# Kernel tuning notes

Measured on AMD Instinct MI355X. Metric: run time of the kernel, lower is better.

The kernel has to match this reference:

```python
import jax, jax.numpy as jnp
import numpy as np
from jax import lax
import math

D_MODEL = 768
D_SSM = 1536      # expand * d_model
D_STATE = 128
D_CONV = 4
HEADDIM = 64
NHEADS = D_SSM // HEADDIM          # 24
CONV_DIM = D_SSM + 2 * D_STATE     # 1792 (ngroups=1)
D_IN_PROJ = 2 * D_SSM + 2 * D_STATE + NHEADS  # 3352
BATCH, SEQLEN = 4, 2048
EPS = 1e-5


def setup_inputs() -> dict:
    key = jax.random.key(0)
    ks = jax.random.split(key, 10)
    u = jax.random.normal(ks[0], (BATCH, SEQLEN, D_MODEL), dtype=jnp.float32)
    W_in = jax.random.normal(ks[1], (D_IN_PROJ, D_MODEL), dtype=jnp.float32) * (1.0 / math.sqrt(D_MODEL))
    conv_w = jax.random.normal(ks[2], (CONV_DIM, D_CONV), dtype=jnp.float32) * (1.0 / math.sqrt(D_CONV))
    conv_b = jax.random.normal(ks[3], (CONV_DIM,), dtype=jnp.float32) * 0.02
    # dt_bias init as in torch code
    dt = jnp.exp(jax.random.uniform(ks[4], (NHEADS,)) * (math.log(0.1) - math.log(0.001)) + math.log(0.001))
    dt = jnp.clip(dt, 1e-4, None)
    dt_bias = dt + jnp.log(-jnp.expm1(-dt))
    A_log = jnp.log(jax.random.uniform(ks[5], (NHEADS,), minval=1.0, maxval=16.0))
    D = jnp.ones((NHEADS,), dtype=jnp.float32)
    norm_w = jnp.ones((D_SSM,), dtype=jnp.float32)
    W_out = jax.random.normal(ks[6], (D_MODEL, D_SSM), dtype=jnp.float32) * (1.0 / math.sqrt(D_SSM))
    return {"u": u, "W_in": W_in, "conv_w": conv_w, "conv_b": conv_b,
            "dt_bias": dt_bias, "A_log": A_log, "D": D, "norm_w": norm_w, "W_out": W_out}


def _mamba2(u, W_in, conv_w, conv_b, dt_bias, A_log, D, norm_w, W_out):
    B_, L, _ = u.shape
    zxbcdt = jnp.einsum('bld,ed->ble', u, W_in)  # [B, L, 3352]
    z = zxbcdt[..., :D_SSM]
    xBC = zxbcdt[..., D_SSM:D_SSM + CONV_DIM]
    dt_raw = zxbcdt[..., D_SSM + CONV_DIM:]      # [B, L, H]

    # causal depthwise conv1d + silu
    xBC_t = jnp.transpose(xBC, (0, 2, 1))        # [B, C, L]
    conv = lax.conv_general_dilated(
        xBC_t, conv_w[:, None, :], window_strides=(1,),
        padding=[(D_CONV - 1, 0)], feature_group_count=CONV_DIM,
        dimension_numbers=('NCH', 'OIH', 'NCH'))
    conv = conv + conv_b[None, :, None]
    xBC = jnp.transpose(jax.nn.silu(conv), (0, 2, 1))  # [B, L, C]

    x = xBC[..., :D_SSM].reshape(B_, L, NHEADS, HEADDIM)
    Bm = xBC[..., D_SSM:D_SSM + D_STATE]         # [B, L, N] (ngroups=1)
    Cm = xBC[..., D_SSM + D_STATE:]              # [B, L, N]

    dt = jax.nn.softplus(dt_raw + dt_bias)       # [B, L, H]
    A = -jnp.exp(A_log)                          # [H]

    def step(h, inp):
        dt_t, x_t, B_t, C_t = inp                # [B,H], [B,H,P], [B,N], [B,N]
        dA = jnp.exp(dt_t * A)                   # [B,H]
        h = h * dA[..., None, None] + jnp.einsum('bh,bhp,bn->bhpn', dt_t, x_t, B_t)
        y_t = jnp.einsum('bhpn,bn->bhp', h, C_t)
        return h, y_t

    h0 = jnp.zeros((B_, NHEADS, HEADDIM, D_STATE), dtype=u.dtype)
    xs = (jnp.transpose(dt, (1, 0, 2)), jnp.transpose(x, (1, 0, 2, 3)),
          jnp.transpose(Bm, (1, 0, 2)), jnp.transpose(Cm, (1, 0, 2)))
    _, ys = lax.scan(step, h0, xs)               # ys: [L, B, H, P]
    y = jnp.transpose(ys, (1, 0, 2, 3)) + D[None, None, :, None] * x
    y = y.reshape(B_, L, D_SSM)

    # RMSNormGated with norm_before_gate=False: normalize after gating
    yz = y * jax.nn.silu(z)
    yn = yz * lax.rsqrt(jnp.mean(yz * yz, axis=-1, keepdims=True) + EPS) * norm_w
    return jnp.einsum('ble,de->bld', yn, W_out)  # [B, L, d_model]


def reference(u, W_in, conv_w, conv_b, dt_bias, A_log, D, norm_w, W_out):
    return _mamba2(u, W_in, conv_w, conv_b, dt_bias, A_log, D, norm_w, W_out)
```

## Files before the change

kernel.cpp:

```cpp
#include <hip/hip_runtime.h>
#include <hip/hip_bf16.h>
#include <math.h>

#define D_MODEL   768
#define D_SSM     1536
#define D_STATE   128
#define D_CONV    4
#define HEADDIM   64
#define NHEADS    24
#define CONV_DIM  1792
#define D_IN_PROJ 3352
#define BATCH     4
#define SEQLEN    2048
#define NROWS     (BATCH * SEQLEN)
#define EPS       1e-5f

#define CHUNK     64
#define NC        (SEQLEN / CHUNK)
#define NBH       (BATCH * NHEADS)
#define HSTATE    (HEADDIM * D_STATE)

#define K3_IN     (3 * D_MODEL)
#define K3_OUT    (3 * D_SSM)
#define NPAD_IN   3456

typedef __attribute__((ext_vector_type(8))) short bf16x8;
typedef __attribute__((ext_vector_type(4))) float f32x4;

__device__ __forceinline__ float sigmoidf_(float x) {
    return 1.0f / (1.0f + __expf(-x));
}

__device__ __forceinline__ void gload16(void* lds, const void* g) {
    __builtin_amdgcn_global_load_lds(
        (const __attribute__((address_space(1))) unsigned int*)g,
        (__attribute__((address_space(3))) unsigned int*)lds, 16, 0, 0);
}

__device__ __forceinline__ void cvt_wr8(__hip_bfloat16* hb, __hip_bfloat16* lb,
                                        int off, float4 a, float4 b)
{
    union { __hip_bfloat16 h[8]; uint4 u; } hi, lo;
    const float f[8] = {a.x, a.y, a.z, a.w, b.x, b.y, b.z, b.w};
#pragma unroll
    for (int j = 0; j < 8; ++j) {
        const __hip_bfloat16 h = __float2bfloat16(f[j]);
        hi.h[j] = h;
        lo.h[j] = __float2bfloat16(f[j] - __bfloat162float(h));
    }
    *(uint4*)((char*)hb + off) = hi.u;
    *(uint4*)((char*)lb + off) = lo.u;
}

template<int APAT>
__global__ __launch_bounds__(256) void decompose3(
    const float* __restrict__ X, __hip_bfloat16* __restrict__ X3,
    int R, int Rpad, int K)
{
    const int idx = blockIdx.x * 256 + threadIdx.x;
    if (idx >= Rpad * (K / 4)) return;
    const int r = idx / (K / 4);
    const int k = (idx % (K / 4)) * 4;

    union { __hip_bfloat16 h[4]; uint2 u; } phi, plo;
    if (r < R) {
        const float4 x = *(const float4*)(X + (size_t)r * K + k);
        const float xs[4] = {x.x, x.y, x.z, x.w};
#pragma unroll
        for (int j = 0; j < 4; ++j) {
            phi.h[j] = __float2bfloat16(xs[j]);
            plo.h[j] = __float2bfloat16(xs[j] - __bfloat162float(phi.h[j]));
        }
    } else {
#pragma unroll
        for (int j = 0; j < 4; ++j) { phi.h[j] = __float2bfloat16(0.f); plo.h[j] = phi.h[j]; }
    }
    __hip_bfloat16* row = X3 + (size_t)r * (3 * K);
    *(uint2*)(row + k)         = phi.u;
    *(uint2*)(row + K + k)     = APAT ? phi.u : plo.u;
    *(uint2*)(row + 2 * K + k) = APAT ? plo.u : phi.u;
}

template<int MODE>
__global__ __launch_bounds__(256) void gemm_bf16x3(
    const __hip_bfloat16* __restrict__ Ab, const __hip_bfloat16* __restrict__ Bb,
    float* __restrict__ C0, float* __restrict__ C1, float* __restrict__ C2,
    int Nreal, int K3)
{
    __shared__ __hip_bfloat16 Asm[2][128][32];
    __shared__ __hip_bfloat16 Bsm[2][128][32];
    const int tid  = threadIdx.x;
    const int lane = tid & 63;
    const int w    = tid >> 6;
    const int wr   = w >> 1, wc = w & 1;
    const int bm   = blockIdx.y * 128;
    const int bn   = blockIdx.x * 128;

    const __hip_bfloat16* gA[2];
    const __hip_bfloat16* gB[2];
    int ldsrow[2];
#pragma unroll
    for (int i = 0; i < 2; ++i) {
        const int r  = w * 32 + i * 16 + (lane >> 2);
        const int sl = (lane & 3) ^ ((r ^ (r >> 2)) & 3);
        ldsrow[i] = w * 32 + i * 16;
        gA[i] = Ab + (size_t)(bm + r) * K3 + sl * 8;
        gB[i] = Bb + (size_t)(bn + r) * K3 + sl * 8;
    }

    int aoff[4], boff[4];
#pragma unroll
    for (int mi = 0; mi < 4; ++mi) {
        const int ra = wr * 64 + mi * 16 + (lane & 15);
        aoff[mi] = ra * 64 + (((lane >> 4) ^ ((ra ^ (ra >> 2)) & 3)) << 4);
        const int rb = wc * 64 + mi * 16 + (lane & 15);
        boff[mi] = rb * 64 + (((lane >> 4) ^ ((rb ^ (rb >> 2)) & 3)) << 4);
    }

    f32x4 acc[4][4] = {};

    const int nk = K3 / 32;
#pragma unroll
    for (int i = 0; i < 2; ++i) {
        gload16(&Asm[0][ldsrow[i]][0], gA[i]);
        gload16(&Bsm[0][ldsrow[i]][0], gB[i]);
    }
    __syncthreads();

    int buf = 0;
    for (int kt = 0; kt < nk; ++kt) {
        if (kt + 1 < nk) {
            const int ko = (kt + 1) * 32;
#pragma unroll
            for (int i = 0; i < 2; ++i) {
                gload16(&Asm[buf ^ 1][ldsrow[i]][0], gA[i] + ko);
                gload16(&Bsm[buf ^ 1][ldsrow[i]][0], gB[i] + ko);
            }
        }
        const char* ab = (const char*)&Asm[buf][0][0];
        const char* bb = (const char*)&Bsm[buf][0][0];
        bf16x8 afr[4], bfr[4];
#pragma unroll
        for (int i = 0; i < 4; ++i) {
            afr[i] = *(const bf16x8*)(ab + aoff[i]);
            bfr[i] = *(const bf16x8*)(bb + boff[i]);
        }
#pragma unroll
        for (int mi = 0; mi < 4; ++mi)
#pragma unroll
            for (int ni = 0; ni < 4; ++ni)
                acc[mi][ni] = __builtin_amdgcn_mfma_f32_16x16x32_bf16(
                    afr[mi], bfr[ni], acc[mi][ni], 0, 0, 0);
        __syncthreads();
        buf ^= 1;
    }

#pragma unroll
    for (int mi = 0; mi < 4; ++mi) {
        const int rn = bm + wr * 64 + mi * 16 + ((lane >> 4) << 2);
#pragma unroll
        for (int ni = 0; ni < 4; ++ni) {
            const int cn = bn + wc * 64 + ni * 16 + (lane & 15);
#pragma unroll
            for (int j = 0; j < 4; ++j) {
                const float v = acc[mi][ni][j];
                const int r = rn + j;
                if (MODE == 0) {
                    C0[(size_t)r * Nreal + cn] = v;
                } else {
                    if (cn < D_SSM)                 C0[(size_t)r * D_SSM + cn] = v;
                    else if (cn < D_SSM + CONV_DIM) C1[(size_t)r * CONV_DIM + (cn - D_SSM)] = v;
                    else if (cn < D_IN_PROJ)        C2[(size_t)r * NHEADS + (cn - D_SSM - CONV_DIM)] = v;
                }
            }
        }
    }
}

template<int BM, int BN, int BK>
__global__ __launch_bounds__(256) void gemm_nt(
    const float* __restrict__ A, const float* __restrict__ B,
    float* __restrict__ C, int M, int N, int K)
{
    __shared__ float As[BK][BM];
    __shared__ float Bs[BK][BN];
    const int tid = threadIdx.x;
    const int bm  = blockIdx.y * BM;
    const int bn  = blockIdx.x * BN;
    const int tm  = (tid & 15) << 2;
    const int tn  = (tid >> 4) << 2;
    const int am  = tid & 63;
    const int ak  = (tid >> 6) << 2;
    float acc[4][4] = {};
    for (int k0 = 0; k0 < K; k0 += BK) {
        const float4 av = *(const float4*)(A + (size_t)(bm + am) * K + (k0 + ak));
        float4 bv = make_float4(0.f, 0.f, 0.f, 0.f);
        if (bn + am < N)
            bv = *(const float4*)(B + (size_t)(bn + am) * K + (k0 + ak));
        __syncthreads();
        As[ak + 0][am] = av.x; As[ak + 1][am] = av.y;
        As[ak + 2][am] = av.z; As[ak + 3][am] = av.w;
        Bs[ak + 0][am] = bv.x; Bs[ak + 1][am] = bv.y;
        Bs[ak + 2][am] = bv.z; Bs[ak + 3][am] = bv.w;
        __syncthreads();
#pragma unroll
        for (int kk = 0; kk < BK; ++kk) {
            const float4 a4 = *(const float4*)&As[kk][tm];
            const float4 b4 = *(const float4*)&Bs[kk][tn];
            const float a[4]  = {a4.x, a4.y, a4.z, a4.w};
            const float bb[4] = {b4.x, b4.y, b4.z, b4.w};
#pragma unroll
            for (int i = 0; i < 4; ++i)
#pragma unroll
                for (int j = 0; j < 4; ++j)
                    acc[i][j] = fmaf(a[i], bb[j], acc[i][j]);
        }
    }
#pragma unroll
    for (int i = 0; i < 4; ++i)
#pragma unroll
        for (int j = 0; j < 4; ++j) {
            const int cn = bn + tn + j;
            if (cn < N)
                C[(size_t)(bm + tm + i) * N + cn] = acc[i][j];
        }
}

__global__ __launch_bounds__(256) void gemm_inproj(
    const float* __restrict__ A, const float* __restrict__ B,
    float* __restrict__ zbuf, float* __restrict__ xbc, float* __restrict__ dtraw)
{
    constexpr int BM = 64, BN = 64, BK = 16;
    __shared__ float As[BK][BM];
    __shared__ float Bs[BK][BN];
    const int tid = threadIdx.x;
    const int bm  = blockIdx.y * BM;
    const int bn  = blockIdx.x * BN;
    const int tm  = (tid & 15) << 2;
    const int tn  = (tid >> 4) << 2;
    const int am  = tid & 63;
    const int ak  = (tid >> 6) << 2;
    float acc[4][4] = {};
    for (int k0 = 0; k0 < D_MODEL; k0 += BK) {
        const float4 av = *(const float4*)(A + (size_t)(bm + am) * D_MODEL + (k0 + ak));
        float4 bv = make_float4(0.f, 0.f, 0.f, 0.f);
        if (bn + am < D_IN_PROJ)
            bv = *(const float4*)(B + (size_t)(bn + am) * D_MODEL + (k0 + ak));
        __syncthreads();
        As[ak + 0][am] = av.x; As[ak + 1][am] = av.y;
        As[ak + 2][am] = av.z; As[ak + 3][am] = av.w;
        Bs[ak + 0][am] = bv.x; Bs[ak + 1][am] = bv.y;
        Bs[ak + 2][am] = bv.z; Bs[ak + 3][am] = bv.w;
        __syncthreads();
#pragma unroll
        for (int kk = 0; kk < BK; ++kk) {
            const float4 a4 = *(const float4*)&As[kk][tm];
            const float4 b4 = *(const float4*)&Bs[kk][tn];
            const float a[4]  = {a4.x, a4.y, a4.z, a4.w};
            const float bb[4] = {b4.x, b4.y, b4.z, b4.w};
#pragma unroll
            for (int i = 0; i < 4; ++i)
#pragma unroll
                for (int j = 0; j < 4; ++j)
                    acc[i][j] = fmaf(a[i], bb[j], acc[i][j]);
        }
    }
    float* Cp; int ldc, cb, nlim = BN;
    if (bn < D_SSM)                  { Cp = zbuf;  ldc = D_SSM;    cb = bn; }
    else if (bn < D_SSM + CONV_DIM)  { Cp = xbc;   ldc = CONV_DIM; cb = bn - D_SSM; }
    else { Cp = dtraw; ldc = NHEADS; cb = bn - (D_SSM + CONV_DIM); nlim = NHEADS; }
#pragma unroll
    for (int i = 0; i < 4; ++i)
#pragma unroll
        for (int j = 0; j < 4; ++j)
            if (tn + j < nlim)
                Cp[(size_t)(bm + tm + i) * ldc + cb + tn + j] = acc[i][j];
}

__global__ __launch_bounds__(256) void conv_silu_kernel(
    const float* __restrict__ xbc, const float* __restrict__ cw,
    const float* __restrict__ cb, float* __restrict__ xc)
{
    const int idx = blockIdx.x * 256 + threadIdx.x;
    if (idx >= NROWS * (CONV_DIM / 4)) return;
    const int row = idx / (CONV_DIM / 4);
    const int c   = (idx % (CONV_DIM / 4)) * 4;
    const int l   = row & (SEQLEN - 1);

    const float* base = xbc + (size_t)row * CONV_DIM + c;
    const float4 cbv = *(const float4*)(cb + c);
    float acc[4] = {cbv.x, cbv.y, cbv.z, cbv.w};
    const float* w = cw + (size_t)c * D_CONV;
#pragma unroll
    for (int k = 0; k < D_CONV; ++k) {
        const int ls = l + k - 3;
        if (ls >= 0) {
            const float4 xv = *(const float4*)(base + (ptrdiff_t)(k - 3) * CONV_DIM);
            acc[0] = fmaf(w[0 * D_CONV + k], xv.x, acc[0]);
            acc[1] = fmaf(w[1 * D_CONV + k], xv.y, acc[1]);
            acc[2] = fmaf(w[2 * D_CONV + k], xv.z, acc[2]);
            acc[3] = fmaf(w[3 * D_CONV + k], xv.w, acc[3]);
        }
    }
    float4 o;
    o.x = acc[0] * sigmoidf_(acc[0]);
    o.y = acc[1] * sigmoidf_(acc[1]);
    o.z = acc[2] * sigmoidf_(acc[2]);
    o.w = acc[3] * sigmoidf_(acc[3]);
    *(float4*)(xc + (size_t)row * CONV_DIM + c) = o;
}

__global__ __launch_bounds__(64) void dt_kernel(
    const float* __restrict__ dtraw, const float* __restrict__ dt_bias,
    float* __restrict__ dtw)
{
    const int row = blockIdx.x;
    const int tid = threadIdx.x;
    if (tid < NHEADS) {
        const float x = dtraw[(size_t)row * NHEADS + tid] + dt_bias[tid];
        const float sp = fmaxf(x, 0.f) + log1pf(__expf(-fabsf(x)));
        dtw[(size_t)row * NHEADS + tid] = sp;
    }
}

__global__ __launch_bounds__(256) void chunk_state_kernel(
    const float* __restrict__ xc, const float* __restrict__ dtw,
    const float* __restrict__ A_log,
    float* __restrict__ Sbuf, float* __restrict__ cumws)
{
    const int c  = blockIdx.x / NBH;
    const int bh = blockIdx.x % NBH;
    const int b  = bh / NHEADS, h = bh % NHEADS;
    const int tid = threadIdx.x;
    const int rowbase = b * SEQLEN + c * CHUNK;

    __shared__ float cums[CHUNK];
    __shared__ float wls[CHUNK];
    __shared__ float Xw[CHUNK][HEADDIM];
    __shared__ float Bsh[CHUNK][D_STATE];

    const float Aneg = -__expf(A_log[h]);

    float dtv = 0.f;
    if (tid < CHUNK) dtv = dtw[(size_t)(rowbase + tid) * NHEADS + h];
    float v = Aneg * dtv;
#pragma unroll
    for (int d = 1; d < 64; d <<= 1) {
        const float o = __shfl_up(v, d);
        if ((tid & 63) >= d) v += o;
    }
    if (tid < CHUNK) {
        cums[tid] = v;
        cumws[(size_t)bh * SEQLEN + c * CHUNK + tid] = v;
    }
    __syncthreads();
    const float clast = cums[CHUNK - 1];
    if (tid < CHUNK) wls[tid] = __expf(clast - v) * dtv;
    __syncthreads();

    {
        const int p0 = (tid & 15) * 4, s0 = tid >> 4;
        for (int s = s0; s < CHUNK; s += 16) {
            const float4 xv = *(const float4*)(xc + (size_t)(rowbase + s) * CONV_DIM + h * HEADDIM + p0);
            const float w = wls[s];
            *(float4*)&Xw[s][p0] = make_float4(xv.x * w, xv.y * w, xv.z * w, xv.w * w);
        }
        const int n0 = (tid & 31) * 4, s1 = tid >> 5;
        for (int s = s1; s < CHUNK; s += 8)
            *(float4*)&Bsh[s][n0] = *(const float4*)(xc + (size_t)(rowbase + s) * CONV_DIM + D_SSM + n0);
    }
    __syncthreads();

    const int tp = (tid & 15) * 4;
    const int tn = (tid >> 4) * 8;
    float acc[4][8] = {};
    for (int s = 0; s < CHUNK; ++s) {
        const float4 xa = *(const float4*)&Xw[s][tp];
        const float4 b0 = *(const float4*)&Bsh[s][tn];
        const float4 b1 = *(const float4*)&Bsh[s][tn + 4];
        const float xr[4] = {xa.x, xa.y, xa.z, xa.w};
        const float br[8] = {b0.x, b0.y, b0.z, b0.w, b1.x, b1.y, b1.z, b1.w};
#pragma unroll
        for (int i = 0; i < 4; ++i)
#pragma unroll
            for (int j = 0; j < 8; ++j)
                acc[i][j] = fmaf(xr[i], br[j], acc[i][j]);
    }
    float* Sp = Sbuf + (size_t)(bh * NC + c) * HSTATE;
#pragma unroll
    for (int i = 0; i < 4; ++i) {
        *(float4*)(Sp + (size_t)(tp + i) * D_STATE + tn)     = make_float4(acc[i][0], acc[i][1], acc[i][2], acc[i][3]);
        *(float4*)(Sp + (size_t)(tp + i) * D_STATE + tn + 4) = make_float4(acc[i][4], acc[i][5], acc[i][6], acc[i][7]);
    }
}

__global__ __launch_bounds__(256) void state_scan_kernel(
    const float* __restrict__ cumws, float* __restrict__ Sbuf)
{
    const int bh = blockIdx.x;
    const int e  = blockIdx.y * 256 + threadIdx.x;
    float* base = Sbuf + (size_t)bh * NC * HSTATE + e;
    const float* cw = cumws + (size_t)bh * SEQLEN;
    float H = 0.f;
    for (int c = 0; c < NC; ++c) {
        const float P = __expf(cw[c * CHUNK + CHUNK - 1]);
        const float s = base[(size_t)c * HSTATE];
        base[(size_t)c * HSTATE] = H;
        H = fmaf(P, H, s);
    }
}

__global__ __launch_bounds__(256) void chunk_output_mfma(
    const float* __restrict__ xc, const float* __restrict__ dtw,
    const float* __restrict__ Dp,
    const float* __restrict__ Hbuf, const float* __restrict__ cumws,
    float* __restrict__ y)
{
    const int c  = blockIdx.x / NBH;
    const int bh = blockIdx.x % NBH;
    const int b  = bh / NHEADS, h = bh % NHEADS;
    const int tid  = threadIdx.x;
    const int lane = tid & 63;
    const int w    = tid >> 6;
    const int rowbase = b * SEQLEN + c * CHUNK;

    __shared__ float s_cums[CHUNK], s_dts[CHUNK], s_Es[CHUNK];
    __shared__ __align__(16) __hip_bfloat16 Chi[CHUNK][D_STATE];
    __shared__ __align__(16) __hip_bfloat16 Clo[CHUNK][D_STATE];
    __shared__ __align__(16) __hip_bfloat16 BHhi[CHUNK][D_STATE];
    __shared__ __align__(16) __hip_bfloat16 BHlo[CHUNK][D_STATE];
    __shared__ __align__(16) __hip_bfloat16 Mhi[CHUNK][CHUNK];
    __shared__ __align__(16) __hip_bfloat16 Mlo[CHUNK][CHUNK];
    __shared__ __align__(16) __hip_bfloat16 XThi[CHUNK][CHUNK];
    __shared__ __align__(16) __hip_bfloat16 XTlo[CHUNK][CHUNK];

    float4 cv[4][2], bvv[4][2];
#pragma unroll
    for (int k = 0; k < 4; ++k) {
        const int q = tid + k * 256;
        const int row = q >> 4, slot = q & 15;
        const float* rp = xc + (size_t)(rowbase + row) * CONV_DIM + D_SSM;
        bvv[k][0] = *(const float4*)(rp + slot * 8);
        bvv[k][1] = *(const float4*)(rp + slot * 8 + 4);
        cv[k][0]  = *(const float4*)(rp + D_STATE + slot * 8);
        cv[k][1]  = *(const float4*)(rp + D_STATE + slot * 8 + 4);
    }
    if (tid < CHUNK) {
        const float cu = cumws[(size_t)bh * SEQLEN + c * CHUNK + tid];
        s_cums[tid] = cu;
        s_Es[tid]   = __expf(cu);
        s_dts[tid]  = dtw[(size_t)(rowbase + tid) * NHEADS + h];
    }
#pragma unroll
    for (int k = 0; k < 4; ++k) {
        const int q = tid + k * 256;
        const int row = q >> 4, slot = q & 15;
        const int off = row * 256 + ((slot ^ (row & 7)) << 4);
        cvt_wr8(&Chi[0][0],  &Clo[0][0],  off, cv[k][0],  cv[k][1]);
        cvt_wr8(&BHhi[0][0], &BHlo[0][0], off, bvv[k][0], bvv[k][1]);
    }
    float4 hv[4][2];
#pragma unroll
    for (int k = 0; k < 4; ++k) {
        const int q = tid + k * 256;
        const int p = q >> 4, slot = q & 15;
        const float* hp = Hbuf + (size_t)(bh * NC + c) * HSTATE + (size_t)p * D_STATE + slot * 8;
        hv[k][0] = *(const float4*)hp;
        hv[k][1] = *(const float4*)(hp + 4);
    }
    float4 xv[4];
#pragma unroll
    for (int k = 0; k < 4; ++k) {
        const int q = tid + k * 256;
        const int s = q >> 4, p4 = (q & 15) * 4;
        xv[k] = *(const float4*)(xc + (size_t)(rowbase + s) * CONV_DIM + h * HEADDIM + p4);
    }
    __syncthreads();

    const int fr = lane & 15;
    const int fs = lane >> 4;
    const int rA = w * 16 + fr;

    f32x4 g[4] = {};
#pragma unroll
    for (int pass = 0; pass < 3; ++pass) {
        const char* Ab = (const char*)(pass == 2 ? &Clo[0][0]  : &Chi[0][0]);
        const char* Bb = (const char*)(pass == 1 ? &BHlo[0][0] : &BHhi[0][0]);
#pragma unroll
        for (int kt = 0; kt < 4; ++kt) {
            const bf16x8 af = *(const bf16x8*)(Ab + rA * 256 + (((kt * 4 + fs) ^ (rA & 7)) << 4));
#pragma unroll
            for (int nt = 0; nt < 4; ++nt) {
                const int rb = nt * 16 + fr;
                const bf16x8 bf = *(const bf16x8*)(Bb + rb * 256 + (((kt * 4 + fs) ^ (rb & 7)) << 4));
                g[nt] = __builtin_amdgcn_mfma_f32_16x16x32_bf16(af, bf, g[nt], 0, 0, 0);
            }
        }
    }

    const float Dh = Dp[h];
#pragma unroll
    for (int nt = 0; nt < 4; ++nt) {
        const int s = nt * 16 + fr;
#pragma unroll
        for (int j = 0; j < 4; ++j) {
            const int t = w * 16 + fs * 4 + j;
            float m = 0.f;
            if (s <= t) {
                m = g[nt][j] * __expf(s_cums[t] - s_cums[s]) * s_dts[s];
                if (s == t) m += Dh;
            }
            const __hip_bfloat16 mh = __float2bfloat16(m);
            const __hip_bfloat16 ml = __float2bfloat16(m - __bfloat162float(mh));
            const int moff = t * 128 + ((((s >> 3) ^ (t & 7))) << 4) + ((s & 7) << 1);
            *(__hip_bfloat16*)((char*)&Mhi[0][0] + moff) = mh;
            *(__hip_bfloat16*)((char*)&Mlo[0][0] + moff) = ml;
        }
    }
    __syncthreads();

#pragma unroll
    for (int k = 0; k < 4; ++k) {
        const int q = tid + k * 256;
        const int p = q >> 4, slot = q & 15;
        const int off = p * 256 + ((slot ^ (p & 7)) << 4);
        cvt_wr8(&BHhi[0][0], &BHlo[0][0], off, hv[k][0], hv[k][1]);
    }
#pragma unroll
    for (int k = 0; k < 4; ++k) {
        const int q = tid + k * 256;
        const int s = q >> 4, p4 = (q & 15) * 4;
        const float f[4] = {xv[k].x, xv[k].y, xv[k].z, xv[k].w};
#pragma unroll
        for (int j = 0; j < 4; ++j) {
            const int p = p4 + j;
            const __hip_bfloat16 xh = __float2bfloat16(f[j]);
            const __hip_bfloat16 xl = __float2bfloat16(f[j] - __bfloat162float(xh));
            const int off = p * 128 + ((((s >> 3) ^ (p & 7))) << 4) + ((s & 7) << 1);
            *(__hip_bfloat16*)((char*)&XThi[0][0] + off) = xh;
            *(__hip_bfloat16*)((char*)&XTlo[0][0] + off) = xl;
        }
    }
    __syncthreads();

    f32x4 acc[4] = {};
#pragma unroll
    for (int pass = 0; pass < 3; ++pass) {
        const char* Ab = (const char*)(pass == 2 ? &Clo[0][0]  : &Chi[0][0]);
        const char* Bb = (const char*)(pass == 1 ? &BHlo[0][0] : &BHhi[0][0]);
#pragma unroll
        for (int kt = 0; kt < 4; ++kt) {
            const bf16x8 af = *(const bf16x8*)(Ab + rA * 256 + (((kt * 4 + fs) ^ (rA & 7)) << 4));
#pragma unroll
            for (int nt = 0; nt < 4; ++nt) {
                const int rp = nt * 16 + fr;
                const bf16x8 bf = *(const bf16x8*)(Bb + rp * 256 + (((kt * 4 + fs) ^ (rp & 7)) << 4));
                acc[nt] = __builtin_amdgcn_mfma_f32_16x16x32_bf16(af, bf, acc[nt], 0, 0, 0);
            }
        }
    }
#pragma unroll
    for (int nt = 0; nt < 4; ++nt)
#pragma unroll
        for (int j = 0; j < 4; ++j)
            acc[nt][j] *= s_Es[w * 16 + fs * 4 + j];

    const int rM = w * 16 + fr;
#pragma unroll
    for (int pass = 0; pass < 3; ++pass) {
        const char* Ab = (const char*)(pass == 2 ? &Mlo[0][0]  : &Mhi[0][0]);
        const char* Bb = (const char*)(pass == 1 ? &XTlo[0][0] : &XThi[0][0]);
#pragma unroll
        for (int kt = 0; kt < 2; ++kt) {
            const bf16x8 af = *(const bf16x8*)(Ab + rM * 128 + (((kt * 4 + fs) ^ (rM & 7)) << 4));
#pragma unroll
            for (int nt = 0; nt < 4; ++nt) {
                const int rp = nt * 16 + fr;
                const bf16x8 bf = *(const bf16x8*)(Bb + rp * 128 + (((kt * 4 + fs) ^ (rp & 7)) << 4));
                acc[nt] = __builtin_amdgcn_mfma_f32_16x16x32_bf16(af, bf, acc[nt], 0, 0, 0);
            }
        }
    }

#pragma unroll
    for (int nt = 0; nt < 4; ++nt) {
        const int p = nt * 16 + fr;
#pragma unroll
        for (int j = 0; j < 4; ++j) {
            const int t = w * 16 + fs * 4 + j;
            y[(size_t)(rowbase + t) * D_SSM + h * HEADDIM + p] = acc[nt][j];
        }
    }
}

__global__ __launch_bounds__(256) void scan_kernel(
    const float* __restrict__ xc, const float* __restrict__ dtw,
    const float* __restrict__ A_log, const float* __restrict__ Dp,
    float* __restrict__ y)
{
    const int b   = blockIdx.x / NHEADS;
    const int h   = blockIdx.x % NHEADS;
    const int tid = threadIdx.x;
    const int p   = tid >> 2;
    const int q   = tid & 3;

    __shared__ float dt_s[SEQLEN];
    __shared__ float Bs[4][36];
    __shared__ float Cs[4][36];
    __shared__ float xs[64];

    for (int i = tid; i < SEQLEN; i += 256)
        dt_s[i] = dtw[((size_t)b * SEQLEN + i) * NHEADS + h];

    const float Aneg = -__expf(A_log[h]);
    const float Dh   = Dp[h];

    float hst[32];
#pragma unroll
    for (int i = 0; i < 32; ++i) hst[i] = 0.f;

    const float* row0 = xc + (size_t)b * SEQLEN * CONV_DIM;
    float rBC = row0[D_SSM + tid];
    float rx  = (tid < 64) ? row0[h * HEADDIM + tid] : 0.f;

    for (int t = 0; t < SEQLEN; ++t) {
        __syncthreads();
        if (tid < 128) Bs[tid >> 5][tid & 31] = rBC;
        else           Cs[(tid >> 5) & 3][tid & 31] = rBC;
        if (tid < 64)  xs[tid] = rx;
        if (t + 1 < SEQLEN) {
            const float* rp = row0 + (size_t)(t + 1) * CONV_DIM;
            rBC = rp[D_SSM + tid];
            if (tid < 64) rx = rp[h * HEADDIM + tid];
        }
        __syncthreads();

        const float dtv = dt_s[t];
        const float dA  = __expf(dtv * Aneg);
        const float dtx = dtv * xs[p];
        float ysum = 0.f;
#pragma unroll
        for (int j4 = 0; j4 < 8; ++j4) {
            const float4 Bv = *(const float4*)&Bs[q][j4 * 4];
            const float4 Cv = *(const float4*)&Cs[q][j4 * 4];
            float* hp = &hst[j4 * 4];
            hp[0] = fmaf(hp[0], dA, dtx * Bv.x); ysum = fmaf(hp[0], Cv.x, ysum);
            hp[1] = fmaf(hp[1], dA, dtx * Bv.y); ysum = fmaf(hp[1], Cv.y, ysum);
            hp[2] = fmaf(hp[2], dA, dtx * Bv.z); ysum = fmaf(hp[2], Cv.z, ysum);
            hp[3] = fmaf(hp[3], dA, dtx * Bv.w); ysum = fmaf(hp[3], Cv.w, ysum);
        }
        ysum += __shfl_xor(ysum, 1);
        ysum += __shfl_xor(ysum, 2);
        if (q == 0)
            y[((size_t)b * SEQLEN + t) * D_SSM + h * HEADDIM + p] = ysum + Dh * xs[p];
    }
}

__global__ __launch_bounds__(256) void gatenorm_x3_kernel(
    const float* __restrict__ y, const float* __restrict__ zbuf,
    const float* __restrict__ norm_w, __hip_bfloat16* __restrict__ ybx3)
{
    const int row = blockIdx.x;
    const int tid = threadIdx.x;
    const float* yr = y + (size_t)row * D_SSM;
    const float* zr = zbuf + (size_t)row * D_SSM;

    float v[6];
    float ss = 0.f;
#pragma unroll
    for (int i = 0; i < 6; ++i) {
        const int e = tid + i * 256;
        const float yv = yr[e];
        const float zv = zr[e];
        const float g  = yv * (zv * sigmoidf_(zv));
        v[i] = g;
        ss = fmaf(g, g, ss);
    }
#pragma unroll
    for (int m = 1; m < 64; m <<= 1) ss += __shfl_xor(ss, m);
    __shared__ float ws[4];
    if ((tid & 63) == 0) ws[tid >> 6] = ss;
    __syncthreads();
    const float tot = ws[0] + ws[1] + ws[2] + ws[3];
    const float r = rsqrtf(tot * (1.0f / D_SSM) + EPS);
    __hip_bfloat16* orow = ybx3 + (size_t)row * K3_OUT;
#pragma unroll
    for (int i = 0; i < 6; ++i) {
        const int e = tid + i * 256;
        const float g = v[i] * r * norm_w[e];
        const __hip_bfloat16 hi = __float2bfloat16(g);
        const __hip_bfloat16 lo = __float2bfloat16(g - __bfloat162float(hi));
        orow[e] = hi;
        orow[D_SSM + e] = hi;
        orow[2 * D_SSM + e] = lo;
    }
}

__global__ __launch_bounds__(256) void gatenorm_kernel(
    float* y, const float* __restrict__ zbuf, const float* __restrict__ norm_w)
{
    const int row = blockIdx.x;
    const int tid = threadIdx.x;
    float* yr = y + (size_t)row * D_SSM;
    const float* zr = zbuf + (size_t)row * D_SSM;

    float v[6];
    float ss = 0.f;
#pragma unroll
    for (int i = 0; i < 6; ++i) {
        const int e = tid + i * 256;
        const float yv = yr[e];
        const float zv = zr[e];
        const float g  = yv * (zv * sigmoidf_(zv));
        v[i] = g;
        ss = fmaf(g, g, ss);
    }
#pragma unroll
    for (int m = 1; m < 64; m <<= 1) ss += __shfl_xor(ss, m);
    __shared__ float ws[4];
    if ((tid & 63) == 0) ws[tid >> 6] = ss;
    __syncthreads();
    const float tot = ws[0] + ws[1] + ws[2] + ws[3];
    const float r = rsqrtf(tot * (1.0f / D_SSM) + EPS);
#pragma unroll
    for (int i = 0; i < 6; ++i) {
        const int e = tid + i * 256;
        yr[e] = v[i] * r * norm_w[e];
    }
}

extern "C" void kernel_launch(void* const* d_in, const int* in_sizes, int n_in,
                              void* d_out, int out_size, void* d_ws, size_t ws_size,
                              hipStream_t stream)
{
    const float* u       = (const float*)d_in[0];
    const float* W_in    = (const float*)d_in[1];
    const float* conv_w  = (const float*)d_in[2];
    const float* conv_b  = (const float*)d_in[3];
    const float* dt_bias = (const float*)d_in[4];
    const float* A_log   = (const float*)d_in[5];
    const float* Dp      = (const float*)d_in[6];
    const float* norm_w  = (const float*)d_in[7];
    const float* W_out   = (const float*)d_in[8];
    float* out = (float*)d_out;

    const size_t SZ_Z   = (size_t)NROWS * D_SSM;
    const size_t SZ_XBC = (size_t)NROWS * CONV_DIM;
    const size_t SZ_DT  = (size_t)NROWS * NHEADS;
    const size_t SZ_S   = (size_t)NBH * NC * HSTATE;
    const size_t SZ_CUM = (size_t)NBH * SEQLEN;

    const size_t need_new = (SZ_Z + SZ_S + SZ_Z + SZ_XBC + SZ_DT + SZ_CUM) * sizeof(float);
    const bool use_new = ws_size >= need_new;

    if (use_new) {
        float* zbuf = (float*)d_ws;
        float* Breg = zbuf + SZ_Z;
        float* Creg = Breg + SZ_S;
        float* Xreg = Creg + SZ_Z;
        float* dtw   = Xreg + SZ_XBC;
        float* cumws = dtw + SZ_DT;

        float* xbc   = Breg;
        float* dtraw = Breg + SZ_XBC;
        float* Sbuf  = Breg;
        __hip_bfloat16* ybx3 = (__hip_bfloat16*)Breg;
        __hip_bfloat16* u3   = (__hip_bfloat16*)Creg;
        float* yb    = Creg;
        __hip_bfloat16* W_in3  = (__hip_bfloat16*)Xreg;
        float* xc    = Xreg;
        __hip_bfloat16* W_out3 = (__hip_bfloat16*)Xreg;

        decompose3<1><<<(NROWS * (D_MODEL / 4) + 255) / 256, 256, 0, stream>>>(
            u, u3, NROWS, NROWS, D_MODEL);
        decompose3<0><<<(NPAD_IN * (D_MODEL / 4) + 255) / 256, 256, 0, stream>>>(
            W_in, W_in3, D_IN_PROJ, NPAD_IN, D_MODEL);

        gemm_bf16x3<1><<<dim3(NPAD_IN / 128, NROWS / 128), 256, 0, stream>>>(
            u3, W_in3, zbuf, xbc, dtraw, 0, K3_IN);

        conv_silu_kernel<<<(NROWS * (CONV_DIM / 4) + 255) / 256, 256, 0, stream>>>(
            xbc, conv_w, conv_b, xc);

        dt_kernel<<<NROWS, 64, 0, stream>>>(dtraw, dt_bias, dtw);

        chunk_state_kernel<<<NBH * NC, 256, 0, stream>>>(xc, dtw, A_log, Sbuf, cumws);
        state_scan_kernel<<<dim3(NBH, HSTATE / 256), 256, 0, stream>>>(cumws, Sbuf);
        chunk_output_mfma<<<NBH * NC, 256, 0, stream>>>(xc, dtw, Dp, Sbuf, cumws, yb);

        decompose3<0><<<(D_MODEL * (D_SSM / 4) + 255) / 256, 256, 0, stream>>>(
            W_out, W_out3, D_MODEL, D_MODEL, D_SSM);

        gatenorm_x3_kernel<<<NROWS, 256, 0, stream>>>(yb, zbuf, norm_w, ybx3);

        gemm_bf16x3<0><<<dim3(D_MODEL / 128, NROWS / 128), 256, 0, stream>>>(
            ybx3, W_out3, out, nullptr, nullptr, D_MODEL, K3_OUT);
    } else {
        float* zbuf  = (float*)d_ws;
        float* Rp    = zbuf + SZ_Z;
        float* xbc   = Rp;
        float* yb    = Rp;
        float* dtraw = Rp + SZ_XBC;
        float* xc    = dtraw + SZ_DT;
        float* dtw   = xc + SZ_XBC;

        gemm_inproj<<<dim3((D_IN_PROJ + 63) / 64, NROWS / 64), 256, 0, stream>>>(
            u, W_in, zbuf, xbc, dtraw);
        conv_silu_kernel<<<(NROWS * (CONV_DIM / 4) + 255) / 256, 256, 0, stream>>>(
            xbc, conv_w, conv_b, xc);
        dt_kernel<<<NROWS, 64, 0, stream>>>(dtraw, dt_bias, dtw);
        scan_kernel<<<NBH, 256, 0, stream>>>(xc, dtw, A_log, Dp, yb);
        gatenorm_kernel<<<NROWS, 256, 0, stream>>>(yb, zbuf, norm_w);
        gemm_nt<64, 64, 16><<<dim3(D_MODEL / 64, NROWS / 64), 256, 0, stream>>>(
            yb, W_out, out, NROWS, D_MODEL, D_SSM);
    }
}
```

Baseline: 727.3 us.

## Use bf16x3 MFMA for chunk state, fuse softplus, swizzle GEMM block order

Replaces the scalar FP32 chunk-state outer-product kernel with a bf16 hi/lo three-pass MFMA version that keeps near-FP32 accuracy. The separate dt softplus kernel is removed; softplus is now recomputed inside the chunk-state and chunk-output kernels, which saves a launch and a buffer round trip. The GEMM grid becomes 1D with a block-index swizzle that spreads consecutive blocks across XCDs, aimed at better L2 locality. Side effects are extra bf16 conversion work and some redundant softplus evaluation.

```diff
diff --git a/kernel.cpp b/kernel.cpp
--- a/kernel.cpp
+++ b/kernel.cpp
@@ -31,6 +31,10 @@
     return 1.0f / (1.0f + __expf(-x));
 }
 
+__device__ __forceinline__ float softplusf_(float x) {
+    return fmaxf(x, 0.f) + log1pf(__expf(-fabsf(x)));
+}
+
 __device__ __forceinline__ void gload16(void* lds, const void* g) {
     __builtin_amdgcn_global_load_lds(
         (const __attribute__((address_space(1))) unsigned int*)g,
@@ -85,7 +89,7 @@
 __global__ __launch_bounds__(256) void gemm_bf16x3(
     const __hip_bfloat16* __restrict__ Ab, const __hip_bfloat16* __restrict__ Bb,
     float* __restrict__ C0, float* __restrict__ C1, float* __restrict__ C2,
-    int Nreal, int K3)
+    int Nreal, int K3, int nx)
 {
     __shared__ __hip_bfloat16 Asm[2][128][32];
     __shared__ __hip_bfloat16 Bsm[2][128][32];
@@ -93,8 +97,11 @@
     const int lane = tid & 63;
     const int w    = tid >> 6;
     const int wr   = w >> 1, wc = w & 1;
-    const int bm   = blockIdx.y * 128;
-    const int bn   = blockIdx.x * 128;
+
+    const int cpx = gridDim.x >> 3;
+    const int swz = (blockIdx.x & 7) * cpx + (blockIdx.x >> 3);
+    const int bm  = (swz / nx) * 128;
+    const int bn  = (swz % nx) * 128;
 
     const __hip_bfloat16* gA[2];
     const __hip_bfloat16* gB[2];
@@ -316,81 +323,123 @@
 {
     const int row = blockIdx.x;
     const int tid = threadIdx.x;
-    if (tid < NHEADS) {
-        const float x = dtraw[(size_t)row * NHEADS + tid] + dt_bias[tid];
-        const float sp = fmaxf(x, 0.f) + log1pf(__expf(-fabsf(x)));
-        dtw[(size_t)row * NHEADS + tid] = sp;
-    }
-}
-
-__global__ __launch_bounds__(256) void chunk_state_kernel(
-    const float* __restrict__ xc, const float* __restrict__ dtw,
-    const float* __restrict__ A_log,
+    if (tid < NHEADS)
+        dtw[(size_t)row * NHEADS + tid] = softplusf_(dtraw[(size_t)row * NHEADS + tid] + dt_bias[tid]);
+}
+
+__global__ __launch_bounds__(256) void chunk_state_mfma(
+    const float* __restrict__ xc, const float* __restrict__ dtraw,
+    const float* __restrict__ dt_bias, const float* __restrict__ A_log,
     float* __restrict__ Sbuf, float* __restrict__ cumws)
 {
     const int c  = blockIdx.x / NBH;
     const int bh = blockIdx.x % NBH;
     const int b  = bh / NHEADS, h = bh % NHEADS;
-    const int tid = threadIdx.x;
+    const int tid  = threadIdx.x;
+    const int lane = tid & 63;
+    const int w    = tid >> 6;
     const int rowbase = b * SEQLEN + c * CHUNK;
 
-    __shared__ float cums[CHUNK];
-    __shared__ float wls[CHUNK];
-    __shared__ float Xw[CHUNK][HEADDIM];
-    __shared__ float Bsh[CHUNK][D_STATE];
-
-    const float Aneg = -__expf(A_log[h]);
-
-    float dtv = 0.f;
-    if (tid < CHUNK) dtv = dtw[(size_t)(rowbase + tid) * NHEADS + h];
-    float v = Aneg * dtv;
-#pragma unroll
-    for (int d = 1; d < 64; d <<= 1) {
-        const float o = __shfl_up(v, d);
-        if ((tid & 63) >= d) v += o;
-    }
+    __shared__ float s_wls[CHUNK];
+    __shared__ __align__(16) __hip_bfloat16 Ahi[CHUNK][CHUNK];
+    __shared__ __align__(16) __hip_bfloat16 Alo[CHUNK][CHUNK];
+    __shared__ __align__(16) __hip_bfloat16 Bhi[D_STATE][CHUNK];
+    __shared__ __align__(16) __hip_bfloat16 Blo[D_STATE][CHUNK];
+
+    float4 bv[8];
+#pragma unroll
+    for (int k = 0; k < 8; ++k) {
+        const int q = tid + k * 256;
+        const int s = q >> 5, n4 = (q & 31) * 4;
+        bv[k] = *(const float4*)(xc + (size_t)(rowbase + s) * CONV_DIM + D_SSM + n4);
+    }
+    float4 xv[4];
+#pragma unroll
+    for (int k = 0; k < 4; ++k) {
+        const int q = tid + k * 256;
+        const int s = q >> 4, p4 = (q & 15) * 4;
+        xv[k] = *(const float4*)(xc + (size_t)(rowbase + s) * CONV_DIM + h * HEADDIM + p4);
+    }
+
     if (tid < CHUNK) {
-        cums[tid] = v;
+        const float Aneg = -__expf(A_log[h]);
+        const float dtv = softplusf_(dtraw[(size_t)(rowbase + tid) * NHEADS + h] + dt_bias[h]);
+        float v = Aneg * dtv;
+#pragma unroll
+        for (int d = 1; d < 64; d <<= 1) {
+            const float o = __shfl_up(v, d);
+            if (lane >= d) v += o;
+        }
         cumws[(size_t)bh * SEQLEN + c * CHUNK + tid] = v;
+        const float clast = __shfl(v, 63);
+        s_wls[tid] = __expf(clast - v) * dtv;
+    }
+
+#pragma unroll
+    for (int k = 0; k < 8; ++k) {
+        const int q = tid + k * 256;
+        const int s = q >> 5, n4 = (q & 31) * 4;
+        const float f[4] = {bv[k].x, bv[k].y, bv[k].z, bv[k].w};
+#pragma unroll
+        for (int j = 0; j < 4; ++j) {
+            const int n = n4 + j;
+            const __hip_bfloat16 hh = __float2bfloat16(f[j]);
+            const __hip_bfloat16 ll = __float2bfloat16(f[j] - __bfloat162float(hh));
+            const int off = n * 128 + ((((s >> 3) ^ (n & 7))) << 4) + ((s & 7) << 1);
+            *(__hip_bfloat16*)((char*)&Bhi[0][0] + off) = hh;
+            *(__hip_bfloat16*)((char*)&Blo[0][0] + off) = ll;
+        }
     }
     __syncthreads();
-    const float clast = cums[CHUNK - 1];
-    if (tid < CHUNK) wls[tid] = __expf(clast - v) * dtv;
+
+#pragma unroll
+    for (int k = 0; k < 4; ++k) {
+        const int q = tid + k * 256;
+        const int s = q >> 4, p4 = (q & 15) * 4;
+        const float wl = s_wls[s];
+        const float f[4] = {xv[k].x * wl, xv[k].y * wl, xv[k].z * wl, xv[k].w * wl};
+#pragma unroll
+        for (int j = 0; j < 4; ++j) {
+            const int p = p4 + j;
+            const __hip_bfloat16 hh = __float2bfloat16(f[j]);
+            const __hip_bfloat16 ll = __float2bfloat16(f[j] - __bfloat162float(hh));
+            const int off = p * 128 + ((((s >> 3) ^ (p & 7))) << 4) + ((s & 7) << 1);
+            *(__hip_bfloat16*)((char*)&Ahi[0][0] + off) = hh;
+            *(__hip_bfloat16*)((char*)&Alo[0][0] + off) = ll;
+        }
+    }
     __syncthreads();
 
-    {
-        const int p0 = (tid & 15) * 4, s0 = tid >> 4;
-        for (int s = s0; s < CHUNK; s += 16) {
-            const float4 xv = *(const float4*)(xc + (size_t)(rowbase + s) * CONV_DIM + h * HEADDIM + p0);
-            const float w = wls[s];
-            *(float4*)&Xw[s][p0] = make_float4(xv.x * w, xv.y * w, xv.z * w, xv.w * w);
-        }
-        const int n0 = (tid & 31) * 4, s1 = tid >> 5;
-        for (int s = s1; s < CHUNK; s += 8)
-            *(float4*)&Bsh[s][n0] = *(const float4*)(xc + (size_t)(rowbase + s) * CONV_DIM + D_SSM + n0);
-    }
-    __syncthreads();
-
-    const int tp = (tid & 15) * 4;
-    const int tn = (tid >> 4) * 8;
-    float acc[4][8] = {};
-    for (int s = 0; s < CHUNK; ++s) {
-        const float4 xa = *(const float4*)&Xw[s][tp];
-        const float4 b0 = *(const float4*)&Bsh[s][tn];
-        const float4 b1 = *(const float4*)&Bsh[s][tn + 4];
-        const float xr[4] = {xa.x, xa.y, xa.z, xa.w};
-        const float br[8] = {b0.x, b0.y, b0.z, b0.w, b1.x, b1.y, b1.z, b1.w};
-#pragma unroll
-        for (int i = 0; i < 4; ++i)
-#pragma unroll
-            for (int j = 0; j < 8; ++j)
-                acc[i][j] = fmaf(xr[i], br[j], acc[i][j]);
-    }
+    const int fr = lane & 15;
+    const int fs = lane >> 4;
+    const int rA = w * 16 + fr;
+    f32x4 acc[8] = {};
+#pragma unroll
+    for (int pass = 0; pass < 3; ++pass) {
+        const char* Ab = (const char*)(pass == 2 ? &Alo[0][0] : &Ahi[0][0]);
+        const char* Bb = (const char*)(pass == 1 ? &Blo[0][0] : &Bhi[0][0]);
+#pragma unroll
+        for (int kh = 0; kh < 2; ++kh) {
+            const int sl = kh * 4 + fs;
+            const bf16x8 af = *(const bf16x8*)(Ab + rA * 128 + ((sl ^ (rA & 7)) << 4));
+#pragma unroll
+            for (int nt = 0; nt < 8; ++nt) {
+                const int rB = nt * 16 + fr;
+                const bf16x8 bf = *(const bf16x8*)(Bb + rB * 128 + ((sl ^ (rB & 7)) << 4));
+                acc[nt] = __builtin_amdgcn_mfma_f32_16x16x32_bf16(af, bf, acc[nt], 0, 0, 0);
+            }
+        }
+    }
+
     float* Sp = Sbuf + (size_t)(bh * NC + c) * HSTATE;
 #pragma unroll
-    for (int i = 0; i < 4; ++i) {
-        *(float4*)(Sp + (size_t)(tp + i) * D_STATE + tn)     = make_float4(acc[i][0], acc[i][1], acc[i][2], acc[i][3]);
-        *(float4*)(Sp + (size_t)(tp + i) * D_STATE + tn + 4) = make_float4(acc[i][4], acc[i][5], acc[i][6], acc[i][7]);
+    for (int nt = 0; nt < 8; ++nt) {
+        const int n = nt * 16 + fr;
+#pragma unroll
+        for (int j = 0; j < 4; ++j) {
+            const int p = w * 16 + fs * 4 + j;
+            Sp[(size_t)p * D_STATE + n] = acc[nt][j];
+        }
     }
 }
 
@@ -411,8 +460,8 @@
 }
 
 __global__ __launch_bounds__(256) void chunk_output_mfma(
-    const float* __restrict__ xc, const float* __restrict__ dtw,
-    const float* __restrict__ Dp,
+    const float* __restrict__ xc, const float* __restrict__ dtraw,
+    const float* __restrict__ dt_bias, const float* __restrict__ Dp,
     const float* __restrict__ Hbuf, const float* __restrict__ cumws,
     float* __restrict__ y)
 {
@@ -449,7 +498,7 @@
         const float cu = cumws[(size_t)bh * SEQLEN + c * CHUNK + tid];
         s_cums[tid] = cu;
         s_Es[tid]   = __expf(cu);
-        s_dts[tid]  = dtw[(size_t)(rowbase + tid) * NHEADS + h];
+        s_dts[tid]  = softplusf_(dtraw[(size_t)(rowbase + tid) * NHEADS + h] + dt_bias[h]);
     }
 #pragma unroll
     for (int k = 0; k < 4; ++k) {
@@ -758,11 +807,10 @@
         float* Breg = zbuf + SZ_Z;
         float* Creg = Breg + SZ_S;
         float* Xreg = Creg + SZ_Z;
-        float* dtw   = Xreg + SZ_XBC;
-        float* cumws = dtw + SZ_DT;
+        float* dtraw = Xreg + SZ_XBC;
+        float* cumws = dtraw + SZ_DT;
 
         float* xbc   = Breg;
-        float* dtraw = Breg + SZ_XBC;
         float* Sbuf  = Breg;
         __hip_bfloat16* ybx3 = (__hip_bfloat16*)Breg;
         __hip_bfloat16* u3   = (__hip_bfloat16*)Creg;
@@ -776,25 +824,25 @@
         decompose3<0><<<(NPAD_IN * (D_MODEL / 4) + 255) / 256, 256, 0, stream>>>(
             W_in, W_in3, D_IN_PROJ, NPAD_IN, D_MODEL);
 
-        gemm_bf16x3<1><<<dim3(NPAD_IN / 128, NROWS / 128), 256, 0, stream>>>(
-            u3, W_in3, zbuf, xbc, dtraw, 0, K3_IN);
+        gemm_bf16x3<1><<<(NPAD_IN / 128) * (NROWS / 128), 256, 0, stream>>>(
+            u3, W_in3, zbuf, xbc, dtraw, 0, K3_IN, NPAD_IN / 128);
 
         conv_silu_kernel<<<(NROWS * (CONV_DIM / 4) + 255) / 256, 256, 0, stream>>>(
             xbc, conv_w, conv_b, xc);
 
-        dt_kernel<<<NROWS, 64, 0, stream>>>(dtraw, dt_bias, dtw);
-
-        chunk_state_kernel<<<NBH * NC, 256, 0, stream>>>(xc, dtw, A_log, Sbuf, cumws);
+        chunk_state_mfma<<<NBH * NC, 256, 0, stream>>>(
+            xc, dtraw, dt_bias, A_log, Sbuf, cumws);
         state_scan_kernel<<<dim3(NBH, HSTATE / 256), 256, 0, stream>>>(cumws, Sbuf);
-        chunk_output_mfma<<<NBH * NC, 256, 0, stream>>>(xc, dtw, Dp, Sbuf, cumws, yb);
+        chunk_output_mfma<<<NBH * NC, 256, 0, stream>>>(
+            xc, dtraw, dt_bias, Dp, Sbuf, cumws, yb);
 
         decompose3<0><<<(D_MODEL * (D_SSM / 4) + 255) / 256, 256, 0, stream>>>(
             W_out, W_out3, D_MODEL, D_MODEL, D_SSM);
 
         gatenorm_x3_kernel<<<NROWS, 256, 0, stream>>>(yb, zbuf, norm_w, ybx3);
 
-        gemm_bf16x3<0><<<dim3(D_MODEL / 128, NROWS / 128), 256, 0, stream>>>(
-            ybx3, W_out3, out, nullptr, nullptr, D_MODEL, K3_OUT);
+        gemm_bf16x3<0><<<(D_MODEL / 128) * (NROWS / 128), 256, 0, stream>>>(
+            ybx3, W_out3, out, nullptr, nullptr, D_MODEL, K3_OUT, D_MODEL / 128);
     } else {
         float* zbuf  = (float*)d_ws;
         float* Rp    = zbuf + SZ_Z;
```

After: 695.6 us. 1.05x faster.
